# Kernel tuning notes

Measured on AMD Instinct MI355X. Metric: run time of the kernel, lower is better.

## Reference

```python
import jax, jax.numpy as jnp
import numpy as np

B, ENC_T, DEC_T = 16, 512, 800
D = 256    # pos_att_dim == att_dim == encoder dim
H = 1024   # attention rnn dim
M = 8      # num gmm mixtures
DELTA_MIN_LIMIT = 0.0
DELTA_OFFSET = 0.0


def setup_inputs() -> dict:
    key = jax.random.key(0)
    ks = jax.random.split(key, 12)
    s = 0.05  # small init so sigmoids/tanh stay in sane range
    b_lin = jnp.concatenate([jnp.zeros((M,)), jnp.zeros((M,)), 3.0 * jnp.ones((M,))])
    return {
        'encoder_outputs': jax.random.normal(ks[0], (B, ENC_T, D), jnp.float32),
        'melenc_outputs': jax.random.normal(ks[1], (B, DEC_T, D), jnp.float32),
        'encoder_lengths': jax.random.randint(ks[2], (B,), ENC_T // 2, ENC_T + 1),
        'output_lengths': jax.random.randint(ks[3], (B,), DEC_T // 2, DEC_T + 1),
        'cond_lens': jax.random.randint(ks[4], (B,), ENC_T // 2, ENC_T + 1),
        'W_ih': jax.random.normal(ks[5], (4 * H, 3 * D), jnp.float32) * s,
        'W_hh': jax.random.normal(ks[6], (4 * H, H), jnp.float32) * s,
        'b_ih': jnp.zeros((4 * H,), jnp.float32),
        'b_hh': jnp.zeros((4 * H,), jnp.float32),
        'W1': jax.random.normal(ks[7], (D, H), jnp.float32) * s,
        'b1': jnp.zeros((D,), jnp.float32),
        'W2': jax.random.normal(ks[8], (D, D), jnp.float32) * s,
        'W_lin': jax.random.normal(ks[9], (3 * M, D), jnp.float32) * 0.01,  # lin.weight.data.mul_(0.01)
        'b_lin': b_lin,
    }


def reference(encoder_outputs, melenc_outputs, encoder_lengths, output_lengths,
              cond_lens, W_ih, W_hh, b_ih, b_hh, W1, b1, W2, W_lin, b_lin):
    Bb, enc_T, Dd = encoder_outputs.shape
    dec_T = melenc_outputs.shape[1]
    n_mix = W_lin.shape[0] // 3
    Hh = W_hh.shape[1]
    dtype = encoder_outputs.dtype

    pos = jnp.arange(enc_T, dtype=dtype)                      # [enc_T]
    cond_f = cond_lens.astype(dtype)
    enc_mask = (pos[None, :] < cond_f[:, None]).astype(dtype)  # [B, enc_T]
    cond_min1 = cond_f - 1.0                                   # [B]
    # dec-step validity mask (get_mask_3d decoder axis), [dec_T, B]
    dec_valid = (jnp.arange(dec_T)[:, None] < output_lengths[None, :]).astype(dtype)

    def lstm_cell(x, h, c):
        g = x @ W_ih.T + b_ih + h @ W_hh.T + b_hh   # [B, 4H]
        i, f, gg, o = jnp.split(g, 4, axis=-1)
        c2 = jax.nn.sigmoid(f) * c + jax.nn.sigmoid(i) * jnp.tanh(gg)
        h2 = jax.nn.sigmoid(o) * jnp.tanh(c2)
        return h2, c2

    def step(carry, xs):
        h, c, ctx, nctx, loc = carry
        mel, vdec = xs                              # mel [B,D], vdec [B]
        q = jnp.concatenate([mel, ctx, nctx], axis=-1)  # [B, 3D]
        h, c = lstm_cell(q, h, c)
        # F network: Linear -> LeakyReLU(0.1) -> Linear(no bias) -> Tanh -> lin
        x = h @ W1.T + b1
        x = jnp.where(x >= 0, x, 0.1 * x)
        x = jnp.tanh(x @ W2.T)
        out = x @ W_lin.T + b_lin                   # [B, 3M]
        w_, d_, s_ = jnp.split(out, 3, axis=-1)
        w = jax.nn.softmax(w_, axis=-1)             # [B, M]
        std = jax.nn.sigmoid(s_)
        delta = jax.nn.sigmoid(d_) + 0.005
        if DELTA_MIN_LIMIT > 0.0:
            delta = jnp.maximum(delta, DELTA_MIN_LIMIT)
        if DELTA_OFFSET > 0.0:
            delta = delta + DELTA_OFFSET
        loc = loc + delta                           # [B, M]
        # tanh-CDF difference over positions: [B, enc_T, M]
        diff = loc[:, None, :] - pos[None, :, None]
        upper = jnp.tanh((diff + 0.5) / std[:, None, :])   # uses pos - 0.5
        lower = jnp.tanh((diff - 0.5) / std[:, None, :])   # uses pos + 0.5
        z = (upper - lower) * 0.5
        align = jnp.einsum('bem,bm->be', z, w)      # [B, enc_T]
        align = align * enc_mask * vdec[:, None]    # masked_fill_(mask, 0.0)
        next_w = jnp.roll(align, 1, axis=-1)
        ctx = jnp.einsum('be,bed->bd', align, encoder_outputs)
        nctx = jnp.einsum('be,bed->bd', next_w, encoder_outputs)
        # loc = loc - (loc - (cond_lens-1)).clamp(min=0)
        loc = loc - jnp.maximum(loc - cond_min1[:, None], 0.0)
        return (h, c, ctx, nctx, loc), (ctx, align)

    init = (jnp.zeros((Bb, Hh), dtype), jnp.zeros((Bb, Hh), dtype),
            jnp.zeros((Bb, Dd), dtype), encoder_outputs[:, 0, :],
            jnp.full((Bb, n_mix), -0.1, dtype))
    xs = (jnp.swapaxes(melenc_outputs, 0, 1), dec_valid)
    _, (ctxs, aligns) = jax.lax.scan(step, init, xs)
    attention_context = jnp.swapaxes(ctxs, 0, 1)    # [B, dec_T, D]
    attention_weights = jnp.swapaxes(aligns, 0, 1)  # [B, dec_T, enc_T]
    # final mask on attention_context over decoder steps
    attention_context = attention_context * jnp.swapaxes(dec_valid, 0, 1)[:, :, None]
    return attention_context, attention_weights
```

## Files before the change

### kernel.cpp

```cpp
#include <hip/hip_runtime.h>
#include <stdint.h>

#define DEV static __device__ __forceinline__

namespace {
constexpr int Bx = 16, ENCx = 512, DECx = 800, Dx = 256, Hx = 1024;
constexpr int NGATE = 128, NCHAIN = 32, NBLK = NGATE + NCHAIN, NTHR = 512;

constexpr int WS_HBH  = 0;
constexpr int WS_CTXH = WS_HBH + 16384;
constexpr int WS_X1M  = WS_CTXH + 8192;
constexpr int WS_FEND = WS_X1M + 8192;
constexpr int IW_HSLOT = 0;
constexpr int IW_XSLOT = 128;
constexpr int IW_CSLOT = 256;
constexpr int IW_HRDY  = 320;
constexpr int IW_XRDY  = 448;
constexpr int IW_CRDY  = 576;
constexpr int IW_END   = 704;
constexpr size_t CTXOUT = (size_t)Bx*DECx*Dx;

constexpr int LH_STR = 1028;
constexpr int CT_STR = 260;
constexpr int LW_H   = 0;
constexpr int LW_WHH = LW_H + 16*LH_STR;
constexpr int LDS_DYN_F = LW_WHH + 16384;
constexpr size_t SMEM_BYTES = (size_t)LDS_DYN_F * 4;
}

DEV float frcp(float x){ return __builtin_amdgcn_rcpf(x); }
DEV float sigm(float x){ return frcp(1.0f + __expf(-x)); }
DEV float ftanh(float x){
  x = fminf(fmaxf(x, -15.0f), 15.0f);
  float e = __expf(2.0f*x);
  return (e - 1.0f) * frcp(e + 1.0f);
}
DEV float wred16(float v){
  v += __shfl_xor(v, 1); v += __shfl_xor(v, 2);
  v += __shfl_xor(v, 4); v += __shfl_xor(v, 8);
  return v;
}
DEV int   ld_rlx(const int* p){ return __hip_atomic_load(p, __ATOMIC_RELAXED, __HIP_MEMORY_SCOPE_AGENT); }
DEV void  st_rlx(int* p, int v){ __hip_atomic_store(p, v, __ATOMIC_RELAXED, __HIP_MEMORY_SCOPE_AGENT); }
DEV void  st_rlx_u32(unsigned* p, unsigned v){ __hip_atomic_store(p, v, __ATOMIC_RELAXED, __HIP_MEMORY_SCOPE_AGENT); }
DEV float ldf_c(const float* p){ return __hip_atomic_load(p, __ATOMIC_RELAXED, __HIP_MEMORY_SCOPE_AGENT); }
DEV void  stf_c(float* p, float v){ __hip_atomic_store(p, v, __ATOMIC_RELAXED, __HIP_MEMORY_SCOPE_AGENT); }
DEV void cbar(){ asm volatile("" ::: "memory"); }

DEV unsigned pack_bf16(float lo, float hi){
  unsigned a = __builtin_bit_cast(unsigned, lo);
  unsigned b = __builtin_bit_cast(unsigned, hi);
  a += 0x7FFFu + ((a >> 16) & 1u);
  b += 0x7FFFu + ((b >> 16) & 1u);
  return (a >> 16) | (b & 0xFFFF0000u);
}
DEV float bflo(unsigned w){ return __builtin_bit_cast(float, w << 16); }
DEV float bfhi(unsigned w){ return __builtin_bit_cast(float, w & 0xFFFF0000u); }

DEV void ld4_wait(float4 (&r)[4], const float* p){
  const float *a1=p+2048,*a2=p+4096,*a3=p+6144;
  asm volatile(
    "global_load_dwordx4 %0, %4, off sc1\n\t"
    "global_load_dwordx4 %1, %5, off sc1\n\t"
    "global_load_dwordx4 %2, %6, off sc1\n\t"
    "global_load_dwordx4 %3, %7, off sc1\n\t"
    "s_waitcnt vmcnt(0)"
    : "=&v"(r[0]),"=&v"(r[1]),"=&v"(r[2]),"=&v"(r[3])
    : "v"(p),"v"(a1),"v"(a2),"v"(a3)
    : "memory");
}
DEV void ld2_wait(float4 (&r)[2], const float* p){
  const float *a1=p+2048;
  asm volatile(
    "global_load_dwordx4 %0, %2, off sc1\n\t"
    "global_load_dwordx4 %1, %3, off sc1\n\t"
    "s_waitcnt vmcnt(0)"
    : "=&v"(r[0]),"=&v"(r[1])
    : "v"(p),"v"(a1)
    : "memory");
}
DEV int4 ld4i_sc1(const int* p){
  int4 r;
  asm volatile("global_load_dwordx4 %0, %1, off sc1\n\ts_waitcnt vmcnt(0)"
    : "=&v"(r) : "v"(p) : "memory");
  return r;
}

DEV void wait_rdy(int* rdy8, int repl, int target, volatile int* lslot){
  const int tid = threadIdx.x;
  if (tid < 64){
    while (ld_rlx(rdy8 + repl*16) < target) __builtin_amdgcn_s_sleep(8);
    if (tid == 0) *lslot = target;
  } else {
    while (*lslot < target) __builtin_amdgcn_s_sleep(1);
  }
  __syncthreads();
  cbar();
}

DEV void detect_pub(int* slots, int nq, int* rdy8, int target, volatile int* lslot){
  const int tid = threadIdx.x;
  if (tid < 64){
    const int* my = slots + tid*4;
    const bool active = (tid < nq);
    for (;;){
      bool ok = true;
      if (active){
        int4 v = ld4i_sc1(my);
        ok = (v.x >= target) & (v.y >= target) & (v.z >= target) & (v.w >= target);
      }
      if (__ballot(ok) == ~0ull) break;
      __builtin_amdgcn_s_sleep(8);
    }
    if (tid < 8) st_rlx(rdy8 + tid*16, target);
    if (tid == 0) *lslot = target;
  } else {
    while (*lslot < target) __builtin_amdgcn_s_sleep(1);
  }
  __syncthreads();
  cbar();
}

extern "C" __global__ void gmm_init(float* wsf){
  int* wsi = (int*)(wsf + WS_FEND);
  int idx = blockIdx.x*blockDim.x + threadIdx.x;
  for (int k = idx; k < IW_END; k += gridDim.x*blockDim.x) wsi[k] = 0;
}

extern "C" __global__ void __launch_bounds__(NTHR, 1) gmm_main(
    const float* __restrict__ enc, const float* __restrict__ mel,
    const int* __restrict__ outlen, const int* __restrict__ condlen,
    const float* __restrict__ Wih, const float* __restrict__ Whh,
    const float* __restrict__ bih, const float* __restrict__ bhh,
    const float* __restrict__ W1,  const float* __restrict__ b1v,
    const float* __restrict__ W2,  const float* __restrict__ Wlin,
    const float* __restrict__ blin,
    float* __restrict__ out, float* __restrict__ wsf)
{
  const int bk = blockIdx.x, tid = threadIdx.x;
  const int klane4 = (tid & 15) * 4;
  const int b4 = (tid >> 4) & 3;
  const int wid = tid >> 6;

  int* wsi   = (int*)(wsf + WS_FEND);
  int* hslot = wsi + IW_HSLOT;
  int* xslot = wsi + IW_XSLOT;
  int* cslot = wsi + IW_CSLOT;
  int* hrdy  = wsi + IW_HRDY;
  int* xrdy  = wsi + IW_XRDY;
  int* crdy  = wsi + IW_CRDY;
  unsigned short* hbh = (unsigned short*)(wsf + WS_HBH);
  unsigned* ctx32u    = (unsigned*)(wsf + WS_CTXH);
  float* x1m = wsf + WS_X1M;

  extern __shared__ float lds[];
  float*    lh      = lds + LW_H;
  unsigned* lwhh_u  = (unsigned*)(lds + LW_WHH);
  const uint2* lwhh2 = (const uint2*)(lds + LW_WHH);

  __shared__ float g_lds[512];
  __shared__ float bsum[32];
  __shared__ float cl[128];
  __shared__ float hstg[128];
  __shared__ float x1l[256];
  __shared__ float x2p[512];
  __shared__ float x2l[256];
  __shared__ float outp[384];
  __shared__ float outl[24];
  __shared__ float mixw[8], mixlc[8], mixis[8];
  __shared__ float locl[8];
  __shared__ float albl[512];
  __shared__ float cpn[2][4][128];
  __shared__ int   s_cond, s_olen;
  __shared__ int   lfh, lfx, lfc;

  if (tid == 0){ lfh = 0; lfx = 0; lfc = 0; }

  const bool is_gate = (bk < NGATE);
  const int  cid = bk - NGATE;
  const int  cb  = cid >> 1;
  const int  hf2 = cid & 1;
  const int  repl = bk & 7;

  const int r0 = wid*4;
  const float* wih[4];
  if (is_gate){
    #pragma unroll
    for (int r = 0; r < 4; ++r){
      int lr = r0 + r;
      wih[r] = Wih + (size_t)((lr>>3)*1024 + bk*8 + (lr&7))*768;
    }
  }

  float4 w2r[32];
  if (is_gate){
    for (int i = tid; i < 16384; i += NTHR){
      int r = i >> 9, c = i & 511;
      size_t gr = (size_t)((r>>3)*1024 + bk*8 + (r&7));
      lwhh_u[i] = pack_bf16(Whh[gr*1024 + 2*c], Whh[gr*1024 + 2*c + 1]);
    }
    if (tid < 32){
      int g = tid >> 3, u = bk*8 + (tid & 7);
      bsum[tid] = bih[g*1024 + u] + bhh[g*1024 + u];
    }
  } else {
    if (tid == 0){ s_cond = condlen[cb]; s_olen = outlen[cb]; }
    if (tid < 8) locl[tid] = -0.1f;
    int r = tid >> 1, hf = tid & 1;
    const float* w2row = W2 + (size_t)r*256 + hf*128;
    #pragma unroll
    for (int i = 0; i < 32; ++i) w2r[i] = *reinterpret_cast<const float4*>(w2row + i*4);
  }
  __syncthreads();

  auto write_h = [&](int t){
    float4 r[4];
    ld4_wait(r, (const float*)(hbh + (t & 1)*16384) + tid*4);
    #pragma unroll
    for (int i = 0; i < 4; ++i){
      unsigned wx = __builtin_bit_cast(unsigned, r[i].x);
      unsigned wy = __builtin_bit_cast(unsigned, r[i].y);
      unsigned wz = __builtin_bit_cast(unsigned, r[i].z);
      unsigned ww = __builtin_bit_cast(unsigned, r[i].w);
      int b = i*4 + (tid >> 7);
      float* d = lh + b*LH_STR + (tid & 127)*8;
      d[0] = bflo(wx); d[1] = bfhi(wx); d[2] = bflo(wy); d[3] = bfhi(wy);
      d[4] = bflo(wz); d[5] = bfhi(wz); d[6] = bflo(ww); d[7] = bfhi(ww);
    }
    __syncthreads();
  };

  auto cell_and_publish = [&](float (&acc)[4][4], int bsel, int stamp, bool first){
    #pragma unroll
    for (int r = 0; r < 4; ++r)
      #pragma unroll
      for (int bi = 0; bi < 4; ++bi){
        float v = wred16(acc[r][bi]);
        if ((tid & 15) == 0) g_lds[(r0 + r)*16 + b4*4 + bi] = v;
      }
    __syncthreads();
    if (tid < 128){
      int u = tid >> 4, b = tid & 15;
      float gi = g_lds[( 0 + u)*16 + b] + bsum[u];
      float gg = g_lds[(16 + u)*16 + b] + bsum[16 + u];
      float go = g_lds[(24 + u)*16 + b] + bsum[24 + u];
      float c2;
      if (first){
        c2 = sigm(gi) * ftanh(gg);
      } else {
        float gf = g_lds[(8 + u)*16 + b] + bsum[8 + u];
        c2 = sigm(gf)*cl[tid] + sigm(gi)*ftanh(gg);
      }
      float h2 = sigm(go)*ftanh(c2);
      cl[tid] = c2;
      hstg[u*16 + b] = h2;
    }
    __syncthreads();
    if (tid < 64){
      int p = tid >> 4, b = tid & 15;
      unsigned w = pack_bf16(hstg[(2*p)*16 + b], hstg[(2*p + 1)*16 + b]);
      st_rlx_u32((unsigned*)hbh + bsel*8192 + b*512 + bk*4 + p, w);
    }
    __syncthreads();
    if (tid == 0) st_rlx(hslot + bk, stamp);
  };

  if (is_gate){
    float acc[4][4] = {};
    #pragma unroll
    for (int it = 0; it < 4; ++it){
      int k = it*64 + klane4;
      float4 wv[4];
      #pragma unroll
      for (int r = 0; r < 4; ++r) wv[r] = *reinterpret_cast<const float4*>(wih[r] + k);
      #pragma unroll
      for (int bi = 0; bi < 4; ++bi){
        float4 xv = *reinterpret_cast<const float4*>(mel + (size_t)(b4*4 + bi)*DECx*Dx + k);
        #pragma unroll
        for (int r = 0; r < 4; ++r)
          acc[r][bi] = fmaf(wv[r].x,xv.x, fmaf(wv[r].y,xv.y, fmaf(wv[r].z,xv.z, fmaf(wv[r].w,xv.w, acc[r][bi]))));
      }
    }
    #pragma unroll
    for (int it = 0; it < 4; ++it){
      int k = it*64 + klane4;
      float4 wv[4];
      #pragma unroll
      for (int r = 0; r < 4; ++r) wv[r] = *reinterpret_cast<const float4*>(wih[r] + 512 + k);
      #pragma unroll
      for (int bi = 0; bi < 4; ++bi){
        float4 xv = *reinterpret_cast<const float4*>(enc + (size_t)(b4*4 + bi)*ENCx*Dx + k);
        #pragma unroll
        for (int r = 0; r < 4; ++r)
          acc[r][bi] = fmaf(wv[r].x,xv.x, fmaf(wv[r].y,xv.y, fmaf(wv[r].z,xv.z, fmaf(wv[r].w,xv.w, acc[r][bi]))));
      }
    }
    cell_and_publish(acc, 0, 1, true);
  }

  for (int t = 0; t < DECx; ++t){
    const int par = t & 1;
    const bool last = (t == DECx - 1);

    if (is_gate){
      if (bk == 0) detect_pub(hslot, 32, hrdy, t + 1, &lfh);
      else         wait_rdy(hrdy, repl, t + 1, &lfh);
      write_h(t);

      {
        int row = tid >> 8;
        int b = (tid >> 4) & 15, kl = tid & 15;
        const float* W1r = W1 + (size_t)(2*bk + row)*1024;
        float a = 0.f;
        #pragma unroll
        for (int it = 0; it < 16; ++it){
          int k = it*64 + kl*4;
          float4 wv = *reinterpret_cast<const float4*>(W1r + k);
          float4 xv = *reinterpret_cast<const float4*>(lh + (size_t)b*LH_STR + k);
          a = fmaf(wv.x,xv.x, fmaf(wv.y,xv.y, fmaf(wv.z,xv.z, fmaf(wv.w,xv.w, a))));
        }
        a = wred16(a);
        if (kl == 0){
          a += b1v[2*bk + row];
          a = (a >= 0.f) ? a : 0.1f*a;
          stf_c(x1m + par*4096 + b*256 + 2*bk + row, a);
        }
      }
      __syncthreads();
      if (tid == 0) st_rlx(xslot + bk, t + 1);

      float acc[4][4] = {};
      if (!last){
        const int tt = t + 1;
        #pragma unroll
        for (int it = 0; it < 4; ++it){
          int k = it*64 + klane4;
          float4 wv[4];
          #pragma unroll
          for (int r = 0; r < 4; ++r) wv[r] = *reinterpret_cast<const float4*>(wih[r] + k);
          #pragma unroll
          for (int bi = 0; bi < 4; ++bi){
            float4 xv = *reinterpret_cast<const float4*>(mel + ((size_t)(b4*4 + bi)*DECx + tt)*Dx + k);
            #pragma unroll
            for (int r = 0; r < 4; ++r)
              acc[r][bi] = fmaf(wv[r].x,xv.x, fmaf(wv[r].y,xv.y, fmaf(wv[r].z,xv.z, fmaf(wv[r].w,xv.w, acc[r][bi]))));
          }
        }
        #pragma unroll 4
        for (int it = 0; it < 16; ++it){
          int k = it*64 + klane4;
          uint2 wv2[4];
          #pragma unroll
          for (int r = 0; r < 4; ++r) wv2[r] = lwhh2[(size_t)(r0 + r)*256 + it*16 + (tid & 15)];
          #pragma unroll
          for (int bi = 0; bi < 4; ++bi){
            float4 xv = *reinterpret_cast<const float4*>(lh + (size_t)(b4*4 + bi)*LH_STR + k);
            #pragma unroll
            for (int r = 0; r < 4; ++r){
              float w0 = bflo(wv2[r].x), w1 = bfhi(wv2[r].x);
              float w2 = bflo(wv2[r].y), w3 = bfhi(wv2[r].y);
              acc[r][bi] = fmaf(w0,xv.x, fmaf(w1,xv.y, fmaf(w2,xv.z, fmaf(w3,xv.w, acc[r][bi]))));
            }
          }
        }
      }

      if (!last){
        if (bk == 0) detect_pub(cslot, 8, crdy, t + 1, &lfc);
        else         wait_rdy(crdy, repl, t + 1, &lfc);
        {
          float4 cr[2];
          ld2_wait(cr, (const float*)(ctx32u + par*4096) + tid*4);
          #pragma unroll
          for (int i = 0; i < 2; ++i){
            unsigned wx = __builtin_bit_cast(unsigned, cr[i].x);
            unsigned wy = __builtin_bit_cast(unsigned, cr[i].y);
            unsigned wz = __builtin_bit_cast(unsigned, cr[i].z);
            unsigned ww = __builtin_bit_cast(unsigned, cr[i].w);
            int base = i*2048 + tid*4;
            int z = base >> 11, b = (base >> 7) & 15, j = base & 127;
            float* d = lh + (z*16 + b)*CT_STR + 2*j;
            d[0] = bflo(wx); d[1] = bfhi(wx); d[2] = bflo(wy); d[3] = bfhi(wy);
            d[4] = bflo(wz); d[5] = bfhi(wz); d[6] = bflo(ww); d[7] = bfhi(ww);
          }
        }
        __syncthreads();
        #pragma unroll
        for (int it = 0; it < 4; ++it){
          int k = it*64 + klane4;
          float4 wv[4];
          #pragma unroll
          for (int r = 0; r < 4; ++r) wv[r] = *reinterpret_cast<const float4*>(wih[r] + 256 + k);
          #pragma unroll
          for (int bi = 0; bi < 4; ++bi){
            float4 xv = *reinterpret_cast<const float4*>(lh + (size_t)(b4*4 + bi)*CT_STR + k);
            #pragma unroll
            for (int r = 0; r < 4; ++r)
              acc[r][bi] = fmaf(wv[r].x,xv.x, fmaf(wv[r].y,xv.y, fmaf(wv[r].z,xv.z, fmaf(wv[r].w,xv.w, acc[r][bi]))));
          }
        }
        #pragma unroll
        for (int it = 0; it < 4; ++it){
          int k = it*64 + klane4;
          float4 wv[4];
          #pragma unroll
          for (int r = 0; r < 4; ++r) wv[r] = *reinterpret_cast<const float4*>(wih[r] + 512 + k);
          #pragma unroll
          for (int bi = 0; bi < 4; ++bi){
            float4 xv = *reinterpret_cast<const float4*>(lh + (size_t)(16 + b4*4 + bi)*CT_STR + k);
            #pragma unroll
            for (int r = 0; r < 4; ++r)
              acc[r][bi] = fmaf(wv[r].x,xv.x, fmaf(wv[r].y,xv.y, fmaf(wv[r].z,xv.z, fmaf(wv[r].w,xv.w, acc[r][bi]))));
          }
        }
        cell_and_publish(acc, (t + 1) & 1, t + 2, false);
      }
    } else {
      if (bk == NGATE) detect_pub(xslot, 32, xrdy, t + 1, &lfx);
      else             wait_rdy(xrdy, repl, t + 1, &lfx);
      if (tid < 256) x1l[tid] = ldf_c(x1m + par*4096 + cb*256 + tid);
      __syncthreads();
      {
        int hf = tid & 1;
        const float* x1b = x1l + hf*128;
        float a = 0.f;
        #pragma unroll
        for (int i = 0; i < 32; ++i){
          float4 xv = *(const float4*)(x1b + i*4);
          a = fmaf(w2r[i].x,xv.x, fmaf(w2r[i].y,xv.y, fmaf(w2r[i].z,xv.z, fmaf(w2r[i].w,xv.w, a))));
        }
        x2p[tid] = a;
      }
      __syncthreads();
      if (tid < 256) x2l[tid] = ftanh(x2p[2*tid] + x2p[2*tid + 1]);
      __syncthreads();
      if (tid < 384){
        int r = tid >> 4, ks = tid & 15;
        const float* wr = Wlin + (size_t)r*256 + ks*16;
        const float* xb = x2l + ks*16;
        float s = 0.f;
        #pragma unroll
        for (int k = 0; k < 16; ++k) s = fmaf(xb[k], wr[k], s);
        outp[tid] = s;
      }
      __syncthreads();
      if (tid < 24){
        float s = blin[tid];
        #pragma unroll
        for (int j = 0; j < 16; ++j) s += outp[tid*16 + j];
        outl[tid] = s;
      }
      __syncthreads();
      if (tid < 8){
        float w = outl[tid];
        float mx = w;
        mx = fmaxf(mx, __shfl_xor(mx, 1)); mx = fmaxf(mx, __shfl_xor(mx, 2)); mx = fmaxf(mx, __shfl_xor(mx, 4));
        float e = __expf(w - mx);
        float sum = e;
        sum += __shfl_xor(sum, 1); sum += __shfl_xor(sum, 2); sum += __shfl_xor(sum, 4);
        mixw[tid] = e * frcp(sum);
        float cm1 = (float)s_cond - 1.0f;
        float dl = sigm(outl[8 + tid]) + 0.005f;
        float lc = locl[tid] + dl;
        mixlc[tid] = lc;
        locl[tid]  = fminf(lc, cm1);
        mixis[tid] = 1.0f + __expf(-outl[16 + tid]);
      }
      __syncthreads();
      {
        float ef = (float)tid;
        float a = 0.f;
        #pragma unroll
        for (int m = 0; m < 8; ++m){
          float df = mixlc[m] - ef;
          a += (ftanh((df + 0.5f)*mixis[m]) - ftanh((df - 0.5f)*mixis[m])) * mixw[m];
        }
        a *= 0.5f;
        bool valid = (tid < s_cond) && (t < s_olen);
        if (!valid) a = 0.f;
        albl[tid] = a;
        if (hf2 == 0)
          out[CTXOUT + (size_t)cb*((size_t)DECx*ENCx) + (size_t)t*ENCx + tid] = a;
      }
      __syncthreads();
      {
        int dl = tid & 127, eg = tid >> 7;
        const float* encb = enc + (size_t)cb*ENCx*Dx + hf2*128;
        float ca = 0.f, na = 0.f;
        #pragma unroll 4
        for (int i = 0; i < 128; ++i){
          int e = eg*128 + i;
          float av = albl[e];
          float nv = albl[(e + 511) & 511];
          float ev = encb[(size_t)e*256 + dl];
          ca = fmaf(av, ev, ca);
          na = fmaf(nv, ev, na);
        }
        cpn[0][eg][dl] = ca;
        cpn[1][eg][dl] = na;
      }
      __syncthreads();
      if (tid < 256){
        int z = tid >> 7, dd = tid & 127;
        float s = cpn[z][0][dd] + cpn[z][1][dd] + cpn[z][2][dd] + cpn[z][3][dd];
        x2p[z*128 + dd] = s;
        if (z == 0)
          out[(size_t)cb*((size_t)DECx*Dx) + (size_t)t*Dx + hf2*128 + dd] = s;
      }
      __syncthreads();
      if (tid < 128){
        int z = tid >> 6, j = tid & 63;
        unsigned w = pack_bf16(x2p[z*128 + 2*j], x2p[z*128 + 2*j + 1]);
        st_rlx_u32(ctx32u + par*4096 + z*2048 + cb*128 + hf2*64 + j, w);
      }
      __syncthreads();
      if (tid == 0) st_rlx(cslot + cid, t + 1);
    }
  }
}

extern "C" void kernel_launch(void* const* d_in, const int* in_sizes, int n_in,
                              void* d_out, int out_size, void* d_ws, size_t ws_size,
                              hipStream_t stream)
{
  const float* enc    = (const float*)d_in[0];
  const float* mel    = (const float*)d_in[1];
  const int*   outlen = (const int*)d_in[3];
  const int*   cond   = (const int*)d_in[4];
  const float* Wih    = (const float*)d_in[5];
  const float* Whh    = (const float*)d_in[6];
  const float* bih    = (const float*)d_in[7];
  const float* bhh    = (const float*)d_in[8];
  const float* W1     = (const float*)d_in[9];
  const float* b1v    = (const float*)d_in[10];
  const float* W2     = (const float*)d_in[11];
  const float* Wlin   = (const float*)d_in[12];
  const float* blin   = (const float*)d_in[13];
  float* outp = (float*)d_out;
  float* wsf  = (float*)d_ws;

  (void)hipFuncSetAttribute((const void*)gmm_main,
                            hipFuncAttributeMaxDynamicSharedMemorySize,
                            (int)SMEM_BYTES);

  hipLaunchKernelGGL(gmm_init, dim3(16), dim3(64), 0, stream, wsf);

  void* args[] = {
    (void*)&enc, (void*)&mel, (void*)&outlen, (void*)&cond,
    (void*)&Wih, (void*)&Whh, (void*)&bih, (void*)&bhh,
    (void*)&W1, (void*)&b1v, (void*)&W2, (void*)&Wlin, (void*)&blin,
    (void*)&outp, (void*)&wsf
  };
  (void)hipLaunchCooperativeKernel((void*)gmm_main, dim3(NBLK), dim3(NTHR),
                                   args, SMEM_BYTES, stream);
}
```

Before: 50.26 ms.

## Move W1 projection from gate blocks into chain blocks with pairwise exchange

The W1·h projection (x1) moves out of the 128 gate blocks and into the 32 chain blocks. Each pair of chain blocks computes half of the 256 rows for its batch element from the bf16 h buffer, then trades halves through a pairwise flag instead of a global xslot detect/publish round. Publishing of the h-ready and ctx-ready flags moves from gate block 0 to chain block 0. This drops one global synchronisation hop per step and takes work off the gate critical path. In exchange, each chain block reads 128 rows of W1 per step from global memory, which adds per-step work to the serial chain path.

```diff
diff --git a/kernel.cpp b/kernel.cpp
--- a/kernel.cpp
+++ b/kernel.cpp
@@ -41,6 +41,7 @@
   return v;
 }
 DEV int   ld_rlx(const int* p){ return __hip_atomic_load(p, __ATOMIC_RELAXED, __HIP_MEMORY_SCOPE_AGENT); }
+DEV unsigned ld_rlx_u32(const unsigned* p){ return __hip_atomic_load(p, __ATOMIC_RELAXED, __HIP_MEMORY_SCOPE_AGENT); }
 DEV void  st_rlx(int* p, int v){ __hip_atomic_store(p, v, __ATOMIC_RELAXED, __HIP_MEMORY_SCOPE_AGENT); }
 DEV void  st_rlx_u32(unsigned* p, unsigned v){ __hip_atomic_store(p, v, __ATOMIC_RELAXED, __HIP_MEMORY_SCOPE_AGENT); }
 DEV float ldf_c(const float* p){ return __hip_atomic_load(p, __ATOMIC_RELAXED, __HIP_MEMORY_SCOPE_AGENT); }
@@ -147,7 +148,6 @@
   int* xslot = wsi + IW_XSLOT;
   int* cslot = wsi + IW_CSLOT;
   int* hrdy  = wsi + IW_HRDY;
-  int* xrdy  = wsi + IW_XRDY;
   int* crdy  = wsi + IW_CRDY;
   unsigned short* hbh = (unsigned short*)(wsf + WS_HBH);
   unsigned* ctx32u    = (unsigned*)(wsf + WS_CTXH);
@@ -162,6 +162,7 @@
   __shared__ float bsum[32];
   __shared__ float cl[128];
   __shared__ float hstg[128];
+  __shared__ float hl[1024];
   __shared__ float x1l[256];
   __shared__ float x2p[512];
   __shared__ float x2l[256];
@@ -173,6 +174,8 @@
   __shared__ float cpn[2][4][128];
   __shared__ int   s_cond, s_olen;
   __shared__ int   lfh, lfx, lfc;
+
+  volatile int* vlfx = &lfx;
 
   if (tid == 0){ lfh = 0; lfx = 0; lfc = 0; }
 
@@ -303,31 +306,8 @@
     const bool last = (t == DECx - 1);
 
     if (is_gate){
-      if (bk == 0) detect_pub(hslot, 32, hrdy, t + 1, &lfh);
-      else         wait_rdy(hrdy, repl, t + 1, &lfh);
+      wait_rdy(hrdy, repl, t + 1, &lfh);
       write_h(t);
-
-      {
-        int row = tid >> 8;
-        int b = (tid >> 4) & 15, kl = tid & 15;
-        const float* W1r = W1 + (size_t)(2*bk + row)*1024;
-        float a = 0.f;
-        #pragma unroll
-        for (int it = 0; it < 16; ++it){
-          int k = it*64 + kl*4;
-          float4 wv = *reinterpret_cast<const float4*>(W1r + k);
-          float4 xv = *reinterpret_cast<const float4*>(lh + (size_t)b*LH_STR + k);
-          a = fmaf(wv.x,xv.x, fmaf(wv.y,xv.y, fmaf(wv.z,xv.z, fmaf(wv.w,xv.w, a))));
-        }
-        a = wred16(a);
-        if (kl == 0){
-          a += b1v[2*bk + row];
-          a = (a >= 0.f) ? a : 0.1f*a;
-          stf_c(x1m + par*4096 + b*256 + 2*bk + row, a);
-        }
-      }
-      __syncthreads();
-      if (tid == 0) st_rlx(xslot + bk, t + 1);
 
       float acc[4][4] = {};
       if (!last){
@@ -366,8 +346,7 @@
       }
 
       if (!last){
-        if (bk == 0) detect_pub(cslot, 8, crdy, t + 1, &lfc);
-        else         wait_rdy(crdy, repl, t + 1, &lfc);
+        wait_rdy(crdy, repl, t + 1, &lfc);
         {
           float4 cr[2];
           ld2_wait(cr, (const float*)(ctx32u + par*4096) + tid*4);
@@ -416,10 +395,55 @@
         cell_and_publish(acc, (t + 1) & 1, t + 2, false);
       }
     } else {
-      if (bk == NGATE) detect_pub(xslot, 32, xrdy, t + 1, &lfx);
-      else             wait_rdy(xrdy, repl, t + 1, &lfx);
-      if (tid < 256) x1l[tid] = ldf_c(x1m + par*4096 + cb*256 + tid);
-      __syncthreads();
+      if (cid == 0) detect_pub(hslot, 32, hrdy, t + 1, &lfh);
+      else          wait_rdy(hrdy, repl, t + 1, &lfh);
+
+      {
+        unsigned w = ld_rlx_u32((unsigned*)hbh + par*8192 + cb*512 + tid);
+        int bkg = tid >> 2, p = tid & 3;
+        hl[bkg*8 + 2*p]     = bflo(w);
+        hl[bkg*8 + 2*p + 1] = bfhi(w);
+      }
+      __syncthreads();
+
+      {
+        int j = tid >> 2, q = tid & 3;
+        int r = hf2*128 + j;
+        const float* W1r = W1 + (size_t)r*1024 + q*256;
+        const float* hq  = hl + q*256;
+        float a = 0.f;
+        #pragma unroll 8
+        for (int i = 0; i < 64; ++i){
+          float4 wv = *reinterpret_cast<const float4*>(W1r + i*4);
+          float4 xv = *reinterpret_cast<const float4*>(hq + i*4);
+          a = fmaf(wv.x,xv.x, fmaf(wv.y,xv.y, fmaf(wv.z,xv.z, fmaf(wv.w,xv.w, a))));
+        }
+        a += __shfl_xor(a, 1);
+        a += __shfl_xor(a, 2);
+        if (q == 0){
+          a += b1v[r];
+          a = (a >= 0.f) ? a : 0.1f*a;
+          x1l[r] = a;
+          stf_c(x1m + par*4096 + cb*256 + r, a);
+        }
+      }
+      __syncthreads();
+      if (tid == 0) st_rlx(xslot + cid, t + 1);
+      if (tid < 64){
+        const int* ps = xslot + (cid ^ 1);
+        while (ld_rlx(ps) < t + 1) __builtin_amdgcn_s_sleep(1);
+        if (tid == 0) *vlfx = t + 1;
+      } else {
+        while (*vlfx < t + 1) __builtin_amdgcn_s_sleep(1);
+      }
+      __syncthreads();
+      cbar();
+      if (tid < 128){
+        int pr = (1 - hf2)*128 + tid;
+        x1l[pr] = ldf_c(x1m + par*4096 + cb*256 + pr);
+      }
+      __syncthreads();
+
       {
         int hf = tid & 1;
         const float* x1b = x1l + hf*128;
@@ -515,6 +539,7 @@
       }
       __syncthreads();
       if (tid == 0) st_rlx(cslot + cid, t + 1);
+      if (cid == 0) detect_pub(cslot, 8, crdy, t + 1, &lfc);
     }
   }
 }
```

After: 52.01 ms. 1.03x slower.

## Pre-convert W_ih and encoder outputs to bf16 workspace copies

Applied to the files above, without the earlier changes.

The init kernel now packs W_ih and the encoder outputs into bf16 buffers in workspace. The gate blocks read W_ih and the chain blocks read encoder values for the context reductions from these buffers, halving bytes per step in the recurrent loop. The x-ready signalling path is also reworked so chain block 0 detects publication into a separate flag slot and then republishes. This trades precision on the weights and encoder values for bandwidth, and adds a one-time conversion pass per call.

```diff
diff --git a/kernel.cpp b/kernel.cpp
--- a/kernel.cpp
+++ b/kernel.cpp
@@ -18,6 +18,9 @@
 constexpr int IW_XRDY  = 448;
 constexpr int IW_CRDY  = 576;
 constexpr int IW_END   = 704;
+constexpr int WS_WIHB = WS_FEND + 768;
+constexpr int WS_ENCB = WS_WIHB + 4096*384;
+constexpr int WS_TOT  = WS_ENCB + 16*512*128;
 constexpr size_t CTXOUT = (size_t)Bx*DECx*Dx;
 
 constexpr int LH_STR = 1028;
@@ -41,6 +44,7 @@
   return v;
 }
 DEV int   ld_rlx(const int* p){ return __hip_atomic_load(p, __ATOMIC_RELAXED, __HIP_MEMORY_SCOPE_AGENT); }
+DEV unsigned ld_rlx_u32(const unsigned* p){ return __hip_atomic_load(p, __ATOMIC_RELAXED, __HIP_MEMORY_SCOPE_AGENT); }
 DEV void  st_rlx(int* p, int v){ __hip_atomic_store(p, v, __ATOMIC_RELAXED, __HIP_MEMORY_SCOPE_AGENT); }
 DEV void  st_rlx_u32(unsigned* p, unsigned v){ __hip_atomic_store(p, v, __ATOMIC_RELAXED, __HIP_MEMORY_SCOPE_AGENT); }
 DEV float ldf_c(const float* p){ return __hip_atomic_load(p, __ATOMIC_RELAXED, __HIP_MEMORY_SCOPE_AGENT); }
@@ -56,6 +60,9 @@
 }
 DEV float bflo(unsigned w){ return __builtin_bit_cast(float, w << 16); }
 DEV float bfhi(unsigned w){ return __builtin_bit_cast(float, w & 0xFFFF0000u); }
+DEV float4 bf4(uint2 w){
+  float4 r; r.x = bflo(w.x); r.y = bfhi(w.x); r.z = bflo(w.y); r.w = bfhi(w.y); return r;
+}
 
 DEV void ld4_wait(float4 (&r)[4], const float* p){
   const float *a1=p+2048,*a2=p+4096,*a3=p+6144;
@@ -121,10 +128,24 @@
   cbar();
 }
 
-extern "C" __global__ void gmm_init(float* wsf){
+extern "C" __global__ void gmm_init(const float* __restrict__ Wih,
+                                    const float* __restrict__ enc,
+                                    float* __restrict__ wsf){
   int* wsi = (int*)(wsf + WS_FEND);
+  unsigned* wihb = (unsigned*)(wsf + WS_WIHB);
+  unsigned* encb = (unsigned*)(wsf + WS_ENCB);
   int idx = blockIdx.x*blockDim.x + threadIdx.x;
-  for (int k = idx; k < IW_END; k += gridDim.x*blockDim.x) wsi[k] = 0;
+  int n = gridDim.x*blockDim.x;
+  for (int k = idx; k < IW_END; k += n) wsi[k] = 0;
+  for (int i = idx; i < 4096*384; i += n){
+    int row = i / 384, c = i % 384;
+    wihb[i] = pack_bf16(Wih[(size_t)row*768 + 2*c], Wih[(size_t)row*768 + 2*c + 1]);
+  }
+  for (int i = idx; i < 16*512*128; i += n){
+    int j = i & 127, e = (i >> 7) & 511, b = i >> 16;
+    const float* s = enc + ((size_t)b*512 + e)*256 + 2*j;
+    encb[i] = pack_bf16(s[0], s[1]);
+  }
 }
 
 extern "C" __global__ void __launch_bounds__(NTHR, 1) gmm_main(
@@ -147,11 +168,12 @@
   int* xslot = wsi + IW_XSLOT;
   int* cslot = wsi + IW_CSLOT;
   int* hrdy  = wsi + IW_HRDY;
-  int* xrdy  = wsi + IW_XRDY;
   int* crdy  = wsi + IW_CRDY;
   unsigned short* hbh = (unsigned short*)(wsf + WS_HBH);
   unsigned* ctx32u    = (unsigned*)(wsf + WS_CTXH);
   float* x1m = wsf + WS_X1M;
+  const unsigned* wsWihB = (const unsigned*)(wsf + WS_WIHB);
+  const unsigned* wsEncB = (const unsigned*)(wsf + WS_ENCB);
 
   extern __shared__ float lds[];
   float*    lh      = lds + LW_H;
@@ -183,12 +205,12 @@
   const int  repl = bk & 7;
 
   const int r0 = wid*4;
-  const float* wih[4];
+  const unsigned* wihb[4];
   if (is_gate){
     #pragma unroll
     for (int r = 0; r < 4; ++r){
       int lr = r0 + r;
-      wih[r] = Wih + (size_t)((lr>>3)*1024 + bk*8 + (lr&7))*768;
+      wihb[r] = wsWihB + (size_t)((lr>>3)*1024 + bk*8 + (lr&7))*384;
     }
   }
 
@@ -272,7 +294,7 @@
       int k = it*64 + klane4;
       float4 wv[4];
       #pragma unroll
-      for (int r = 0; r < 4; ++r) wv[r] = *reinterpret_cast<const float4*>(wih[r] + k);
+      for (int r = 0; r < 4; ++r) wv[r] = bf4(*reinterpret_cast<const uint2*>(wihb[r] + (k>>1)));
       #pragma unroll
       for (int bi = 0; bi < 4; ++bi){
         float4 xv = *reinterpret_cast<const float4*>(mel + (size_t)(b4*4 + bi)*DECx*Dx + k);
@@ -286,7 +308,7 @@
       int k = it*64 + klane4;
       float4 wv[4];
       #pragma unroll
-      for (int r = 0; r < 4; ++r) wv[r] = *reinterpret_cast<const float4*>(wih[r] + 512 + k);
+      for (int r = 0; r < 4; ++r) wv[r] = bf4(*reinterpret_cast<const uint2*>(wihb[r] + 256 + (k>>1)));
       #pragma unroll
       for (int bi = 0; bi < 4; ++bi){
         float4 xv = *reinterpret_cast<const float4*>(enc + (size_t)(b4*4 + bi)*ENCx*Dx + k);
@@ -337,7 +359,7 @@
           int k = it*64 + klane4;
           float4 wv[4];
           #pragma unroll
-          for (int r = 0; r < 4; ++r) wv[r] = *reinterpret_cast<const float4*>(wih[r] + k);
+          for (int r = 0; r < 4; ++r) wv[r] = bf4(*reinterpret_cast<const uint2*>(wihb[r] + (k>>1)));
           #pragma unroll
           for (int bi = 0; bi < 4; ++bi){
             float4 xv = *reinterpret_cast<const float4*>(mel + ((size_t)(b4*4 + bi)*DECx + tt)*Dx + k);
@@ -390,7 +412,7 @@
           int k = it*64 + klane4;
           float4 wv[4];
           #pragma unroll
-          for (int r = 0; r < 4; ++r) wv[r] = *reinterpret_cast<const float4*>(wih[r] + 256 + k);
+          for (int r = 0; r < 4; ++r) wv[r] = bf4(*reinterpret_cast<const uint2*>(wihb[r] + 128 + (k>>1)));
           #pragma unroll
           for (int bi = 0; bi < 4; ++bi){
             float4 xv = *reinterpret_cast<const float4*>(lh + (size_t)(b4*4 + bi)*CT_STR + k);
@@ -404,7 +426,7 @@
           int k = it*64 + klane4;
           float4 wv[4];
           #pragma unroll
-          for (int r = 0; r < 4; ++r) wv[r] = *reinterpret_cast<const float4*>(wih[r] + 512 + k);
+          for (int r = 0; r < 4; ++r) wv[r] = bf4(*reinterpret_cast<const uint2*>(wihb[r] + 256 + (k>>1)));
           #pragma unroll
           for (int bi = 0; bi < 4; ++bi){
             float4 xv = *reinterpret_cast<const float4*>(lh + (size_t)(16 + b4*4 + bi)*CT_STR + k);
@@ -416,8 +438,11 @@
         cell_and_publish(acc, (t + 1) & 1, t + 2, false);
       }
     } else {
-      if (bk == NGATE) detect_pub(xslot, 32, xrdy, t + 1, &lfx);
-      else             wait_rdy(xrdy, repl, t + 1, &lfx);
+      if (cid == 0) detect_pub(xslot, 32, hrdy + 8*16, t + 1, &lfx);
+      else          wait_rdy(wsi + IW_XRDY, repl, t + 1, &lfx);
+      if (cid == 0 && tid < 8) st_rlx(wsi + IW_XRDY + tid*16, t + 1);
+      __syncthreads();
+      cbar();
       if (tid < 256) x1l[tid] = ldf_c(x1m + par*4096 + cb*256 + tid);
       __syncthreads();
       {
@@ -485,14 +510,16 @@
       __syncthreads();
       {
         int dl = tid & 127, eg = tid >> 7;
-        const float* encb = enc + (size_t)cb*ENCx*Dx + hf2*128;
+        const unsigned* encbB = wsEncB + (size_t)cb*(512*128) + hf2*64 + (dl >> 1);
+        const int hi = dl & 1;
         float ca = 0.f, na = 0.f;
         #pragma unroll 4
         for (int i = 0; i < 128; ++i){
           int e = eg*128 + i;
           float av = albl[e];
           float nv = albl[(e + 511) & 511];
-          float ev = encb[(size_t)e*256 + dl];
+          unsigned w = encbB[(size_t)e*128];
+          float ev = hi ? bfhi(w) : bflo(w);
           ca = fmaf(av, ev, ca);
           na = fmaf(nv, ev, na);
         }
@@ -543,7 +570,7 @@
                             hipFuncAttributeMaxDynamicSharedMemorySize,
                             (int)SMEM_BYTES);
 
-  hipLaunchKernelGGL(gmm_init, dim3(16), dim3(64), 0, stream, wsf);
+  hipLaunchKernelGGL(gmm_init, dim3(256), dim3(256), 0, stream, Wih, enc, wsf);
 
   void* args[] = {
     (void*)&enc, (void*)&mel, (void*)&outlen, (void*)&cond,
```

After: 67.96 ms. 1.35x slower.
